# Optimization experiments

Hardware: AMD Instinct MI355X
Metric: run time of the kernel (lower is better)

The kernel has to match this reference:

```python
import jax, jax.numpy as jnp
import numpy as np

B, L, H, V = 256, 4096, 64, 64
LN_EPS = 1e-5


def setup_inputs() -> dict:
    key = jax.random.key(0)
    ks = jax.random.split(key, 12)
    s = 1.0 / np.sqrt(H)
    return {
        "seq": jax.random.randint(ks[0], (B, L), 0, V),
        "embed_W": jax.random.normal(ks[1], (V, H), jnp.float32),
        "ff_w1": jax.random.normal(ks[2], (H, 2 * H), jnp.float32) * s,
        "ff_b1": jnp.zeros((2 * H,), jnp.float32),
        "ff_w2": jax.random.normal(ks[3], (2 * H, H), jnp.float32) * s,
        "ff_b2": jnp.zeros((H,), jnp.float32),
        "ln_w": jnp.ones((H,), jnp.float32),
        "ln_b": jnp.zeros((H,), jnp.float32),
        "read_w": jax.random.normal(ks[4], (H, H), jnp.float32) * s,
        "read_b": jnp.zeros((H,), jnp.float32),
        "out_w": jax.random.normal(ks[5], (H, V), jnp.float32) * s,
        "out_b": jnp.zeros((V,), jnp.float32),
    }


def _layer_norm(x, w, b):
    mu = jnp.mean(x, axis=-1, keepdims=True)
    var = jnp.mean(jnp.square(x - mu), axis=-1, keepdims=True)
    return (x - mu) * jax.lax.rsqrt(var + LN_EPS) * w + b


def reference(seq, embed_W, ff_w1, ff_b1, ff_w2, ff_b2, ln_w, ln_b,
              read_w, read_b, out_w, out_b):
    h = embed_W[seq]  # (B, L, H)
    ff = jax.nn.relu(h @ ff_w1 + ff_b1) @ ff_w2 + ff_b2
    h = _layer_norm(h + ff, ln_w, ln_b)

    def step(M, k):  # M: (B,H,H), k: (B,H)
        v_pred = jnp.einsum('bij,bj->bi', M, k)
        denom = jnp.sum(k * k, axis=-1, keepdims=True) + 1e-6
        dv = k - v_pred / denom
        M = M + dv[:, :, None] * k[:, None, :]  # rank-1 delta write
        return M, None

    ks = jnp.swapaxes(h[:, :-1, :], 0, 1)  # (L-1, B, H)
    M0 = jnp.zeros((h.shape[0], h.shape[-1], h.shape[-1]), h.dtype)
    M, _ = jax.lax.scan(step, M0, ks)

    q = h[:, -1, :]
    ctx = jnp.einsum('bij,bj->bi', M, q)
    return (ctx @ read_w + read_b) @ out_w + out_b  # (B, V)
```

## Files before the change

### kernel.cpp

```cpp
#include <hip/hip_runtime.h>
#include <hip/hip_bf16.h>

#define LN_EPS 1e-5f

static __device__ __forceinline__ float readlane_f(float v, int lane) {
    return __int_as_float(__builtin_amdgcn_readlane(__float_as_int(v), lane));
}
static __device__ __forceinline__ void writelane_f(int& dst, float val, int lane_imm) {
    asm volatile("v_writelane_b32 %0, %1, %2"
                 : "+v"(dst)
                 : "s"(__float_as_int(val)), "i"(lane_imm));
}

__global__ __launch_bounds__(64) void build_keys(
    const float* __restrict__ embed,
    const float* __restrict__ w1,
    const float* __restrict__ b1,
    const float* __restrict__ w2,
    const float* __restrict__ b2,
    const float* __restrict__ lnw,
    const float* __restrict__ lnb,
    float* __restrict__ keytab)
{
    const int v = blockIdx.x, lane = threadIdx.x;
    __shared__ float se[64];
    __shared__ float sh[128];
    se[lane] = embed[v * 64 + lane];
    __syncthreads();
    float h0 = b1[lane];
    float h1 = b1[lane + 64];
    #pragma unroll 8
    for (int i = 0; i < 64; ++i) {
        float e = se[i];
        h0 = fmaf(e, w1[i * 128 + lane], h0);
        h1 = fmaf(e, w1[i * 128 + lane + 64], h1);
    }
    sh[lane]      = fmaxf(h0, 0.f);
    sh[lane + 64] = fmaxf(h1, 0.f);
    __syncthreads();
    float acc = b2[lane];
    #pragma unroll 8
    for (int j = 0; j < 128; ++j)
        acc = fmaf(sh[j], w2[j * 64 + lane], acc);
    float pre = se[lane] + acc;
    float sum = pre;
    #pragma unroll
    for (int off = 32; off >= 1; off >>= 1) sum += __shfl_xor(sum, off, 64);
    float mu  = sum * (1.f / 64.f);
    float dev = pre - mu;
    float sq  = dev * dev;
    #pragma unroll
    for (int off = 32; off >= 1; off >>= 1) sq += __shfl_xor(sq, off, 64);
    float var = sq * (1.f / 64.f);
    float key = dev * (1.f / sqrtf(var + LN_EPS)) * lnw[lane] + lnb[lane];
    keytab[v * 64 + lane] = key;
}

__global__ __launch_bounds__(64) void build_tables(
    const float* __restrict__ keytab,
    const float* __restrict__ read_w,
    const float* __restrict__ read_b,
    const float* __restrict__ out_w,
    const float* __restrict__ out_b,
    float* __restrict__ Gg,
    float* __restrict__ GhatN,
    float* __restrict__ Wc,
    float* __restrict__ biasv)
{
    const int w = blockIdx.x, lane = threadIdx.x;
    __shared__ float sk[64 * 65];
    __shared__ float srw[64];
    #pragma unroll 8
    for (int r = 0; r < 64; ++r) sk[r * 65 + lane] = keytab[r * 64 + lane];
    srw[lane] = read_w[w * 64 + lane];
    __syncthreads();
    float g = 0.f;
    #pragma unroll 8
    for (int i = 0; i < 64; ++i)
        g = fmaf(sk[w * 65 + i], sk[lane * 65 + i], g);
    float gww  = readlane_f(g, w);
    float beta = 1.f / (gww + 1e-6f);
    Gg[w * 64 + lane]    = g;
    GhatN[w * 64 + lane] = -(beta * g);
    float acc = 0.f;
    #pragma unroll 8
    for (int j = 0; j < 64; ++j)
        acc = fmaf(srw[j], out_w[j * 64 + lane], acc);
    Wc[w * 64 + lane] = acc;
    if (w == 0) {
        float bacc = out_b[lane];
        #pragma unroll 8
        for (int j = 0; j < 64; ++j)
            bacc = fmaf(read_b[j], out_w[j * 64 + lane], bacc);
        biasv[lane] = bacc;
    }
}

__global__ __launch_bounds__(64) void delta_scan(
    const int*   __restrict__ seq,
    const float* __restrict__ Gg,
    const float* __restrict__ GhatN,
    const float* __restrict__ keytab,
    const float* __restrict__ Wc,
    const float* __restrict__ biasv,
    float* __restrict__ out)
{
    const int lane = threadIdx.x;
    const int b    = blockIdx.x;
    __shared__ float sG[64 * 64];
    __shared__ float sc[64];
    __shared__ float sCtx[64];
    #pragma unroll 8
    for (int r = 0; r < 64; ++r) sG[r * 64 + lane] = GhatN[r * 64 + lane];
    sc[lane] = 0.f;
    const int* seqb = seq + (size_t)b * 4096;
    float d = Gg[seqb[4095] * 64 + lane];
    __syncthreads();

    int vS = 0;
    int vcur = seqb[64 * 63 + lane];
    int   wq[9];
    float q_[9];
    #pragma unroll
    for (int s = 0; s < 9; ++s) {
        wq[s] = __builtin_amdgcn_readlane(vcur, 62 - s);
        q_[s] = sG[wq[s] * 64 + lane];
    }

    #pragma unroll 1
    for (int blk = 64; blk >= 0; --blk) {
        int vnext = (blk > 0) ? seqb[(blk - 1) * 63 + lane] : vcur;
        #pragma unroll
        for (int j = 62; j >= 0; --j) {
            const int slot = (62 - j) % 9;
            const int jl   = j - 9;
            int   w0 = wq[slot];
            float p  = readlane_f(d, w0);
            d = fmaf(p, q_[slot], d);
            writelane_f(vS, p, j);
            int wn = (jl >= 0) ? __builtin_amdgcn_readlane(vcur, jl)
                               : __builtin_amdgcn_readlane(vnext, jl + 63);
            wq[slot] = wn;
            q_[slot] = sG[wn * 64 + lane];
        }
        atomicAdd(&sc[vcur & 63], __int_as_float(vS));
        vS = 0;
        vcur = vnext;
    }
    __syncthreads();

    float ctx = 0.f;
    #pragma unroll 8
    for (int v = 0; v < 64; ++v)
        ctx = fmaf(sc[v], keytab[v * 64 + lane], ctx);
    sCtx[lane] = ctx;
    __syncthreads();
    float o = biasv[lane];
    #pragma unroll 8
    for (int i = 0; i < 64; ++i)
        o = fmaf(sCtx[i], Wc[i * 64 + lane], o);
    out[(size_t)b * 64 + lane] = o;
}

extern "C" void kernel_launch(void* const* d_in, const int* in_sizes, int n_in,
                              void* d_out, int out_size, void* d_ws, size_t ws_size,
                              hipStream_t stream) {
    const int*   seq    = (const int*)d_in[0];
    const float* embed  = (const float*)d_in[1];
    const float* ff_w1  = (const float*)d_in[2];
    const float* ff_b1  = (const float*)d_in[3];
    const float* ff_w2  = (const float*)d_in[4];
    const float* ff_b2  = (const float*)d_in[5];
    const float* ln_w   = (const float*)d_in[6];
    const float* ln_b   = (const float*)d_in[7];
    const float* read_w = (const float*)d_in[8];
    const float* read_b = (const float*)d_in[9];
    const float* out_w  = (const float*)d_in[10];
    const float* out_b  = (const float*)d_in[11];
    float* out = (float*)d_out;

    float* wsf    = (float*)d_ws;
    float* keytab = wsf;
    float* Gg     = wsf + 4096;
    float* GhatN  = wsf + 8192;
    float* Wc     = wsf + 12288;
    float* biasv  = wsf + 16384;

    build_keys<<<64, 64, 0, stream>>>(embed, ff_w1, ff_b1, ff_w2, ff_b2, ln_w, ln_b, keytab);
    build_tables<<<64, 64, 0, stream>>>(keytab, read_w, read_b, out_w, out_b,
                                        Gg, GhatN, Wc, biasv);
    delta_scan<<<256, 64, 0, stream>>>(seq, Gg, GhatN, keytab, Wc, biasv, out);
}
```

Measured before the change: 175.3 us.

## Block three sequential delta-scan steps to shorten the serial dependency chain

The serial scan over tokens is regrouped so that three consecutive rank-1 updates are handled per group. The three coefficients are read at once, corrected via small precomputed cross terms (Aq), and then applied as three FMAs. This cuts the readlane→FMA critical-path latency per token by resolving intra-group dependencies on scalar-like values rather than through the full vector state. In exchange it adds extra readlanes and selects per group, and it changes floating-point rounding order.

```diff
diff --git a/kernel.cpp b/kernel.cpp
--- a/kernel.cpp
+++ b/kernel.cpp
@@ -5,6 +5,9 @@
 
 static __device__ __forceinline__ float readlane_f(float v, int lane) {
     return __int_as_float(__builtin_amdgcn_readlane(__float_as_int(v), lane));
+}
+static __device__ __forceinline__ float readlane_fs(float v, int slane) {
+    return __int_as_float(__builtin_amdgcn_readlane(__float_as_int(v), slane));
 }
 static __device__ __forceinline__ void writelane_f(int& dst, float val, int lane_imm) {
     asm volatile("v_writelane_b32 %0, %1, %2"
@@ -119,29 +122,56 @@
 
     int vS = 0;
     int vcur = seqb[64 * 63 + lane];
-    int   wq[9];
-    float q_[9];
+    int   wq[3][3];
+    float rq[3][3];
+    float Aq[3][3];
     #pragma unroll
-    for (int s = 0; s < 9; ++s) {
-        wq[s] = __builtin_amdgcn_readlane(vcur, 62 - s);
-        q_[s] = sG[wq[s] * 64 + lane];
-    }
+    for (int s = 0; s < 3; ++s)
+        #pragma unroll
+        for (int k = 0; k < 3; ++k) {
+            wq[s][k] = __builtin_amdgcn_readlane(vcur, 62 - 3 * s - k);
+            rq[s][k] = sG[wq[s][k] * 64 + lane];
+        }
+    Aq[0][0] = readlane_fs(rq[0][0], wq[0][1]);
+    Aq[0][1] = readlane_fs(rq[0][0], wq[0][2]);
+    Aq[0][2] = readlane_fs(rq[0][1], wq[0][2]);
 
     #pragma unroll 1
     for (int blk = 64; blk >= 0; --blk) {
         int vnext = (blk > 0) ? seqb[(blk - 1) * 63 + lane] : vcur;
         #pragma unroll
-        for (int j = 62; j >= 0; --j) {
-            const int slot = (62 - j) % 9;
-            const int jl   = j - 9;
-            int   w0 = wq[slot];
-            float p  = readlane_f(d, w0);
-            d = fmaf(p, q_[slot], d);
-            writelane_f(vS, p, j);
-            int wn = (jl >= 0) ? __builtin_amdgcn_readlane(vcur, jl)
-                               : __builtin_amdgcn_readlane(vnext, jl + 63);
-            wq[slot] = wn;
-            q_[slot] = sG[wn * 64 + lane];
+        for (int gg = 0; gg < 21; ++gg) {
+            const int j     = 62 - 3 * gg;
+            const int slot  = gg % 3;
+            const int nslot = (gg + 1) % 3;
+            const int wa = wq[slot][0], wb = wq[slot][1], wc = wq[slot][2];
+            float p0 = readlane_fs(d, wa);
+            float p1 = readlane_fs(d, wb);
+            float p2 = readlane_fs(d, wc);
+            float s1v = fmaf(Aq[slot][0], p0, p1);
+            float s2v = fmaf(Aq[slot][1], p0, p2);
+            s2v = fmaf(Aq[slot][2], s1v, s2v);
+            d = fmaf(p0,  rq[slot][0], d);
+            d = fmaf(s1v, rq[slot][1], d);
+            d = fmaf(s2v, rq[slot][2], d);
+            writelane_f(vS, p0, j);
+            vS = (lane == j - 1) ? __float_as_int(s1v) : vS;
+            vS = (lane == j - 2) ? __float_as_int(s2v) : vS;
+            Aq[nslot][0] = readlane_fs(rq[nslot][0], wq[nslot][1]);
+            Aq[nslot][1] = readlane_fs(rq[nslot][0], wq[nslot][2]);
+            Aq[nslot][2] = readlane_fs(rq[nslot][1], wq[nslot][2]);
+            {
+                const int jb = j - 9;
+                int wn0 = (jb     >= 0) ? __builtin_amdgcn_readlane(vcur, jb)
+                                        : __builtin_amdgcn_readlane(vnext, jb + 63);
+                int wn1 = (jb - 1 >= 0) ? __builtin_amdgcn_readlane(vcur, jb - 1)
+                                        : __builtin_amdgcn_readlane(vnext, jb + 62);
+                int wn2 = (jb - 2 >= 0) ? __builtin_amdgcn_readlane(vcur, jb - 2)
+                                        : __builtin_amdgcn_readlane(vnext, jb + 61);
+                wq[slot][0] = wn0; rq[slot][0] = sG[wn0 * 64 + lane];
+                wq[slot][1] = wn1; rq[slot][1] = sG[wn1 * 64 + lane];
+                wq[slot][2] = wn2; rq[slot][2] = sG[wn2 * 64 + lane];
+            }
         }
         atomicAdd(&sc[vcur & 63], __int_as_float(vS));
         vS = 0;
```

Result: slower. 201.0 us (+14.7%).

## Break serial readlane dependency in delta scan with lookahead recurrence

Applied to the files above, without the earlier changes.

Restructures the serial scan step so each step's scalar p no longer needs a readlane of the freshly updated d vector. It precomputes readlanes three steps ahead and corrects them with the two most recent step outputs through stored coupling coefficients. This shortens the critical latency chain of readlane→fma→readlane per step, in exchange for more readlane and FMA instructions per step. The lane-select write replaces the writelane asm.

```diff
diff --git a/kernel.cpp b/kernel.cpp
--- a/kernel.cpp
+++ b/kernel.cpp
@@ -120,28 +120,42 @@
     int vS = 0;
     int vcur = seqb[64 * 63 + lane];
     int   wq[9];
-    float q_[9];
+    float rq[9];
     #pragma unroll
     for (int s = 0; s < 9; ++s) {
         wq[s] = __builtin_amdgcn_readlane(vcur, 62 - s);
-        q_[s] = sG[wq[s] * 64 + lane];
-    }
+        rq[s] = sG[wq[s] * 64 + lane];
+    }
+    float rlq[3], A1q[3], A2q[3];
+    rlq[0] = readlane_f(d, wq[0]);
+    rlq[1] = readlane_f(d, wq[1]);
+    rlq[2] = readlane_f(d, wq[2]);
+    A1q[0] = 0.f;                      A2q[0] = 0.f;
+    A1q[1] = readlane_f(rq[0], wq[1]); A2q[1] = 0.f;
+    A1q[2] = readlane_f(rq[1], wq[2]); A2q[2] = readlane_f(rq[0], wq[2]);
+    float sm1 = 0.f, sm2 = 0.f;
 
     #pragma unroll 1
     for (int blk = 64; blk >= 0; --blk) {
         int vnext = (blk > 0) ? seqb[(blk - 1) * 63 + lane] : vcur;
         #pragma unroll
         for (int j = 62; j >= 0; --j) {
-            const int slot = (62 - j) % 9;
-            const int jl   = j - 9;
-            int   w0 = wq[slot];
-            float p  = readlane_f(d, w0);
-            d = fmaf(p, q_[slot], d);
-            writelane_f(vS, p, j);
+            const int ph = (62 - j) % 3;
+            const int rs = (62 - j) % 9;
+            float t0 = fmaf(A2q[ph], sm2, rlq[ph]);
+            float sn = fmaf(A1q[ph], sm1, t0);
+            vS = (lane == j) ? __float_as_int(sn) : vS;
+            int w3 = wq[(rs + 3) % 9];
+            A2q[ph] = readlane_f(rq[(rs + 1) % 9], w3);
+            A1q[ph] = readlane_f(rq[(rs + 2) % 9], w3);
+            d = fmaf(sn, rq[rs], d);
+            rlq[ph] = readlane_f(d, w3);
+            const int jl = j - 9;
             int wn = (jl >= 0) ? __builtin_amdgcn_readlane(vcur, jl)
                                : __builtin_amdgcn_readlane(vnext, jl + 63);
-            wq[slot] = wn;
-            q_[slot] = sG[wn * 64 + lane];
+            wq[rs] = wn;
+            rq[rs] = sG[wn * 64 + lane];
+            sm2 = sm1; sm1 = sn;
         }
         atomicAdd(&sc[vcur & 63], __int_as_float(vS));
         vS = 0;
```

Result: slower. 247.8 us (+41.4%).
